# Kernel optimization log

Measured on AMD Instinct MI355X. Metric: run time of the kernel, lower is better.

## Reference

```python
import jax, jax.numpy as jnp
import numpy as np
import math

B, L, D = 4, 4096, 1024
PI = math.pi
LN_EPS = 1e-5


def setup_inputs() -> dict:
    key = jax.random.key(0)
    ks = jax.random.split(key, 16)
    s = 1.0 / math.sqrt(D)
    inp = {
        "x": jax.random.normal(ks[0], (B, L, D), dtype=jnp.float32),
        # Linear weights stored as [in, out] (torch W.T)
        "Wk": jax.random.normal(ks[1], (D, D), dtype=jnp.float32) * s,
        "bk": jnp.zeros((D,), dtype=jnp.float32),
        "Wq": jax.random.normal(ks[2], (D, D), dtype=jnp.float32) * s,
        "bq": jnp.zeros((D,), dtype=jnp.float32),
        "Wv": jax.random.normal(ks[3], (D, D), dtype=jnp.float32) * s,
        "bv": jnp.zeros((D,), dtype=jnp.float32),
        "ln_g": jnp.ones((D,), dtype=jnp.float32),
        "ln_b": jnp.zeros((D,), dtype=jnp.float32),
        "Wo": jax.random.normal(ks[4], (D, D), dtype=jnp.float32) * s,
        "bo": jnp.zeros((D,), dtype=jnp.float32),
        "Wg1": jax.random.normal(ks[5], (D, D // 4), dtype=jnp.float32) * s,
        "bg1": jnp.zeros((D // 4,), dtype=jnp.float32),
        "Wg2": jax.random.normal(ks[6], (D // 4, 1), dtype=jnp.float32) * (2.0 / math.sqrt(D)),
        "bg2": jnp.zeros((1,), dtype=jnp.float32),
        "pos_phases": jax.random.normal(ks[7], (L, D), dtype=jnp.float32) * PI,
    }
    return inp


def _layernorm(x, g, b):
    mu = jnp.mean(x, axis=-1, keepdims=True)
    var = jnp.var(x, axis=-1, keepdims=True)
    return (x - mu) * jax.lax.rsqrt(var + LN_EPS) * g + b


def reference(x, Wk, bk, Wq, bq, Wv, bv, ln_g, ln_b, Wo, bo, Wg1, bg1, Wg2, bg2, pos_phases):
    # dropout is identity in eval mode
    key_phases = jnp.tanh(x @ Wk + bk) * PI          # [B,L,D]
    query_phases = jnp.tanh(x @ Wq + bq) * PI        # [B,L,D]
    V = x @ Wv + bv                                   # [B,L,D]

    cos_k, sin_k = jnp.cos(key_phases), jnp.sin(key_phases)
    cos_q, sin_q = jnp.cos(query_phases), jnp.sin(query_phases)

    mem_real = jnp.cumsum(V * cos_k, axis=1)
    mem_imag = jnp.cumsum(V * sin_k, axis=1)
    content_retrieved = mem_real * cos_q + mem_imag * sin_q

    pp = pos_phases[: x.shape[1]]                     # [L,D]
    cos_p, sin_p = jnp.cos(pp), jnp.sin(pp)
    pos_mem_real = jnp.cumsum(V * cos_p, axis=1)
    pos_mem_imag = jnp.cumsum(V * sin_p, axis=1)
    pos_retrieved = pos_mem_real * cos_p + pos_mem_imag * sin_p

    gate = jax.nn.sigmoid(jax.nn.gelu(x @ Wg1 + bg1) @ Wg2 + bg2)  # [B,L,1]
    combined = gate * content_retrieved + (1.0 - gate) * pos_retrieved

    positions = jnp.arange(1, x.shape[1] + 1, dtype=jnp.float32)
    norm = jnp.sqrt(positions)[None, :, None]
    out = _layernorm(combined / norm, ln_g, ln_b) @ Wo + bo
    return x + out
```

## Files before the change

kernel.cpp:

```cpp
#include <hip/hip_runtime.h>
#include <math.h>

#define B_ 4
#define L_ 4096
#define D_ 1024
#define DG_ 256
#define NC_ 256
#define CL_ 16
#define SEGL_ 8
#define NSEG_ 32
#define PI_F 3.14159265358979323846f
#define LN_EPS_F 1e-5f

typedef __attribute__((ext_vector_type(8))) _Float16 f16x8;
typedef __attribute__((ext_vector_type(8))) short s16x8;
typedef __attribute__((ext_vector_type(4))) short s16x4;
typedef __attribute__((ext_vector_type(4))) float f32x4;

__device__ inline short f2h(float f) { return __builtin_bit_cast(short, (_Float16)f); }
__device__ inline float h2f(short s) { return (float)__builtin_bit_cast(_Float16, s); }

__device__ inline float ftanh(float x) {
    float e = __expf(2.0f * x);
    return 1.0f - 2.0f / (e + 1.0f);
}
__device__ inline void fsincos(float x, float* s, float* c) {
    *s = __sinf(x); *c = __cosf(x);
}

__device__ inline void gld16(const void* g, void* l) {
    __builtin_amdgcn_global_load_lds(
        (const __attribute__((address_space(1))) unsigned int*)g,
        (__attribute__((address_space(3))) unsigned int*)l, 16, 0, 0);
}

__global__ __launch_bounds__(256)
void conv_x(const float* __restrict__ x, short* __restrict__ xh, int n8)
{
    int t = blockIdx.x * 256 + threadIdx.x;
    if (t >= n8) return;
    const float4* p = (const float4*)x + (size_t)t * 2;
    float4 a = p[0], b = p[1];
    s16x8 v;
    v[0] = f2h(a.x); v[1] = f2h(a.y); v[2] = f2h(a.z); v[3] = f2h(a.w);
    v[4] = f2h(b.x); v[5] = f2h(b.y); v[6] = f2h(b.z); v[7] = f2h(b.w);
    *(s16x8*)(xh + (size_t)t * 8) = v;
}

__global__ __launch_bounds__(256)
void csp_kernel(const float* __restrict__ PP, short* __restrict__ CSP, int n4)
{
    int t = blockIdx.x * 256 + threadIdx.x;
    if (t >= n4) return;
    f32x4 p = *(const f32x4*)&PP[(size_t)t * 4];
    s16x8 o;
    #pragma unroll
    for (int j = 0; j < 4; ++j) {
        float s, c;
        fsincos(p[j], &s, &c);
        o[2 * j] = f2h(c);
        o[2 * j + 1] = f2h(s);
    }
    *(s16x8*)&CSP[(size_t)t * 8] = o;
}

__global__ __launch_bounds__(256)
void convT(const float* __restrict__ W, short* __restrict__ Th, int N)
{
    __shared__ float tile[64][65];
    const int n0 = blockIdx.x * 64, k0 = blockIdx.y * 64;
    const int t = threadIdx.x;
    const int r = t >> 4, c4 = (t & 15) * 4;

    #pragma unroll
    for (int i = 0; i < 4; ++i) {
        float4 v = *(const float4*)&W[(size_t)(k0 + r + i * 16) * N + n0 + c4];
        tile[r + i * 16][c4 + 0] = v.x;
        tile[r + i * 16][c4 + 1] = v.y;
        tile[r + i * 16][c4 + 2] = v.z;
        tile[r + i * 16][c4 + 3] = v.w;
    }
    __syncthreads();
    #pragma unroll
    for (int i = 0; i < 4; ++i) {
        const int n = r + i * 16;
        s16x4 o;
        o[0] = f2h(tile[c4 + 0][n]);
        o[1] = f2h(tile[c4 + 1][n]);
        o[2] = f2h(tile[c4 + 2][n]);
        o[3] = f2h(tile[c4 + 3][n]);
        *(s16x4*)&Th[(size_t)(n0 + n) * 1024 + k0 + c4] = o;
    }
}

#define BARRIER() __builtin_amdgcn_s_barrier()
#define PRIO1() __builtin_amdgcn_s_setprio(1)
#define PRIO0() __builtin_amdgcn_s_setprio(0)
#define LGKM0() do { asm volatile("s_waitcnt lgkmcnt(0)" ::: "memory"); \
                     __builtin_amdgcn_sched_barrier(0); } while (0)
#define VMC(N) asm volatile("s_waitcnt vmcnt(" #N ")" ::: "memory")

#define DSR(dst, areg, OFS)                                              \
    asm volatile("ds_read_b128 %0, %1 offset:" OFS                       \
                 : "=v"(dst) : "v"(areg))

#define RDA4(areg)                                                       \
    DSR(af[0], areg, "0");    DSR(af[1], areg, "2048");                  \
    DSR(af[2], areg, "4096"); DSR(af[3], areg, "6144");
#define RDA4H(areg)                                                      \
    DSR(af[0], areg, "8192");  DSR(af[1], areg, "10240");                \
    DSR(af[2], areg, "12288"); DSR(af[3], areg, "14336");
#define RDB4(areg, KK)                                                   \
    DSR(bq[0][KK], areg, "0");    DSR(bq[1][KK], areg, "2048");          \
    DSR(bq[2][KK], areg, "4096"); DSR(bq[3][KK], areg, "6144");

#define MF(MG, KK)                                                       \
    _Pragma("unroll") for (int i_ = 0; i_ < 4; ++i_)                     \
    _Pragma("unroll") for (int n_ = 0; n_ < 4; ++n_)                     \
        acc[(MG)*4 + i_][n_] = __builtin_amdgcn_mfma_f32_16x16x32_f16(   \
            af[i_], bq[n_][KK], acc[(MG)*4 + i_][n_], 0, 0, 0);

template<int EPI, typename OT>
__global__ __launch_bounds__(512, 2)
void mgemm256(const short* __restrict__ A, const short* __restrict__ Bt,
              const float* __restrict__ X, OT* __restrict__ out0,
              short* __restrict__ out1, short* __restrict__ out2,
              const float* __restrict__ b0, const float* __restrict__ b1,
              const float* __restrict__ b2, int M, int N, int K)
{
    extern __shared__ char lds[];

    const int tid = threadIdx.x;
    const int w = tid >> 6, l = tid & 63;
    const int wr = w >> 2, wc = w & 3;
    const int fr = l & 15, kb = l >> 4;
    const int bm = blockIdx.x * 256, bn = blockIdx.y * 256;
    const int np = K >> 7;

    const int s = fr & 7;
    const int cK0 = (((s >> 2) & 1) << 6) | (((kb ^ s) & 3) << 4);
    const int aA0 = (wr << 14) + fr * 128 + cK0;
    const int aA1 = aA0 ^ 64;
    const int aB0 = 32768 + ((wc >> 1) << 14) + ((wc & 1) * 64 + fr) * 128 + cK0;
    const int aB1 = aB0 ^ 64;
    const int aA0o = aA0 + 65536, aA1o = aA1 + 65536;
    const int aB0o = aB0 + 65536, aB1o = aB1 + 65536;

    const int p0 = tid * 16;
    const int sr = p0 >> 7;
    const int sc = (p0 & 127) ^ ((sr & 7) << 4);
    const short* gA = A  + (size_t)(bm + sr) * K + (sc >> 1);
    const short* gB = Bt + (size_t)(bn + sr) * K + (sc >> 1);
    char* ldst = lds + (w << 10);
    const size_t q1 = (size_t)64 * K, q2 = 2 * q1, q3 = 3 * q1;

    f32x4 acc[8][4] = {};
    f16x8 af[4];
    f16x8 bq[4][2];

    gld16(gA,      ldst);          gld16(gA + q1, ldst + 8192);
    gld16(gA + q2, ldst + 16384);  gld16(gA + q3, ldst + 24576);
    gld16(gB,      ldst + 32768);  gld16(gB + q1, ldst + 40960);
    gld16(gB + q2, ldst + 49152);  gld16(gB + q3, ldst + 57344);
    VMC(0);
    BARRIER();

    const short* gAn = gA + 64;
    const short* gBn = gB + 64;

    for (int pp = 0; pp < np; ++pp) {
        const bool nl = (pp + 1 < np);

        RDA4(aA0); RDB4(aB0, 0);
        gld16(gBn,      ldst + 98304);         gld16(gBn + q1, ldst + 98304 + 8192);
        gld16(gBn + q2, ldst + 98304 + 16384); gld16(gBn + q3, ldst + 98304 + 24576);
        LGKM0();
        PRIO1(); MF(0, 0); PRIO0();
        RDA4(aA1); RDB4(aB1, 1);
        gld16(gAn,      ldst + 65536);         gld16(gAn + q1, ldst + 65536 + 8192);
        gld16(gAn + q2, ldst + 65536 + 16384); gld16(gAn + q3, ldst + 65536 + 24576);
        LGKM0();
        PRIO1(); MF(0, 1); PRIO0();
        RDA4H(aA0);
        LGKM0();
        PRIO1(); MF(1, 0); PRIO0();
        RDA4H(aA1);
        LGKM0();
        PRIO1(); MF(1, 1); PRIO0();
        VMC(0);
        BARRIER();

        RDA4(aA0o); RDB4(aB0o, 0);
        if (nl) {
            gld16(gBn +      64, ldst + 32768); gld16(gBn + q1 + 64, ldst + 40960);
            gld16(gBn + q2 + 64, ldst + 49152); gld16(gBn + q3 + 64, ldst + 57344);
        }
        LGKM0();
        PRIO1(); MF(0, 0); PRIO0();
        RDA4(aA1o); RDB4(aB1o, 1);
        if (nl) {
            gld16(gAn +      64, ldst);         gld16(gAn + q1 + 64, ldst + 8192);
            gld16(gAn + q2 + 64, ldst + 16384); gld16(gAn + q3 + 64, ldst + 24576);
        }
        LGKM0();
        PRIO1(); MF(0, 1); PRIO0();
        RDA4H(aA0o);
        LGKM0();
        PRIO1(); MF(1, 0); PRIO0();
        RDA4H(aA1o);
        LGKM0();
        PRIO1(); MF(1, 1); PRIO0();
        if (nl) {
            VMC(0);
            BARRIER();
        }
        gAn += 128; gBn += 128;
    }

    if constexpr (EPI == 4) {
        short* op; const float* bp; bool dt;
        if (bn < 1024)      { op = (short*)out0; bp = b0; dt = true;  }
        else if (bn < 2048) { op = out1;         bp = b1; dt = true;  }
        else                { op = out2;         bp = b2; dt = false; }
        const int cb = bn & 1023;
        float bc[4];
        #pragma unroll
        for (int nf = 0; nf < 4; ++nf) bc[nf] = bp[cb + wc * 64 + nf * 16 + fr];
        #pragma unroll
        for (int mf = 0; mf < 8; ++mf)
            #pragma unroll
            for (int rr = 0; rr < 4; ++rr) {
                const int row = bm + wr * 128 + mf * 16 + kb * 4 + rr;
                #pragma unroll
                for (int nf = 0; nf < 4; ++nf) {
                    const int cc = cb + wc * 64 + nf * 16 + fr;
                    float c = acc[mf][nf][rr] + bc[nf];
                    if (dt) c = ftanh(c) * PI_F;
                    op[(size_t)row * 1024 + cc] = f2h(c);
                }
            }
    } else {
        float bc[4];
        #pragma unroll
        for (int nf = 0; nf < 4; ++nf) bc[nf] = b0[bn + wc * 64 + nf * 16 + fr];
        #pragma unroll
        for (int mf = 0; mf < 8; ++mf)
            #pragma unroll
            for (int rr = 0; rr < 4; ++rr) {
                const int row = bm + wr * 128 + mf * 16 + kb * 4 + rr;
                #pragma unroll
                for (int nf = 0; nf < 4; ++nf) {
                    const int col = bn + wc * 64 + nf * 16 + fr;
                    float c = acc[mf][nf][rr] + bc[nf] + X[(size_t)row * N + col];
                    ((float*)out0)[(size_t)row * N + col] = c;
                }
            }
    }
}

#define RDAF(areg)                                                       \
    DSR(af[0], areg, "0");    DSR(af[1], areg, "2048");                  \
    DSR(af[2], areg, "4096"); DSR(af[3], areg, "6144");
#define RDBF(areg)                                                       \
    DSR(bqs[0], areg, "0");    DSR(bqs[1], areg, "2048");                \
    DSR(bqs[2], areg, "4096"); DSR(bqs[3], areg, "6144");

#define MF16()                                                           \
    _Pragma("unroll") for (int i_ = 0; i_ < 4; ++i_)                     \
    _Pragma("unroll") for (int n_ = 0; n_ < 4; ++n_)                     \
        acc[i_][n_] = __builtin_amdgcn_mfma_f32_16x16x32_f16(            \
            af[i_], bqs[n_], acc[i_][n_], 0, 0, 0);

template<int EPI>
__global__ __launch_bounds__(256, 2)
void gemm128(const short* __restrict__ A, const short* __restrict__ Bt,
             const float* __restrict__ b0, const float* __restrict__ wg2p,
             float* __restrict__ gatep, int M, int N, int K)
{
    extern __shared__ char lds[];

    const int tid = threadIdx.x;
    const int w = tid >> 6, l = tid & 63;
    const int wr = w >> 1, wc = w & 1;
    const int fr = l & 15, kb = l >> 4;
    const int bm = blockIdx.x * 128, bn = blockIdx.y * 128;

    const int s = fr & 7;
    const int cK0 = (((s >> 2) & 1) << 6) | (((kb ^ s) & 3) << 4);
    const int aA0e = (wr * 64 + fr) * 128 + cK0;
    const int aA1e = aA0e ^ 64;
    const int aB0e = 16384 + (wc * 64 + fr) * 128 + cK0;
    const int aB1e = aB0e ^ 64;
    const int aA0o = aA0e + 32768, aA1o = aA1e + 32768;
    const int aB0o = aB0e + 32768, aB1o = aB1e + 32768;

    const int p16 = tid * 16;
    const int sr = p16 >> 7;
    const int sc = (p16 & 127) ^ ((sr & 7) << 4);
    const short* gA = A  + (size_t)(bm + sr) * K + (sc >> 1);
    const short* gB = Bt + (size_t)(bn + sr) * K + (sc >> 1);
    char* ldA = lds + (w << 10);
    const size_t r32 = (size_t)32 * K;

    f32x4 acc[4][4] = {};
    f16x8 af[4], bqs[4];

    #pragma unroll
    for (int i = 0; i < 4; ++i) gld16(gA + i * r32, ldA + i * 4096);
    #pragma unroll
    for (int i = 0; i < 4; ++i) gld16(gB + i * r32, ldA + 16384 + i * 4096);
    VMC(0);
    BARRIER();

    const short* gAt = gA;
    const short* gBt = gB;
    const int np = K >> 7;

    for (int pp = 0; pp < np; ++pp) {
        const bool nl = (pp + 1 < np);

        RDAF(aA0e); RDBF(aB0e);
        #pragma unroll
        for (int i = 0; i < 4; ++i) gld16(gAt + 64 + i * r32, ldA + 32768 + i * 4096);
        LGKM0();
        PRIO1(); MF16(); PRIO0();
        RDAF(aA1e); RDBF(aB1e);
        #pragma unroll
        for (int i = 0; i < 4; ++i) gld16(gBt + 64 + i * r32, ldA + 49152 + i * 4096);
        LGKM0();
        PRIO1(); MF16(); PRIO0();
        VMC(0);
        BARRIER();

        RDAF(aA0o); RDBF(aB0o);
        if (nl) {
            #pragma unroll
            for (int i = 0; i < 4; ++i) gld16(gAt + 128 + i * r32, ldA + i * 4096);
        }
        LGKM0();
        PRIO1(); MF16(); PRIO0();
        RDAF(aA1o); RDBF(aB1o);
        if (nl) {
            #pragma unroll
            for (int i = 0; i < 4; ++i) gld16(gBt + 128 + i * r32, ldA + 16384 + i * 4096);
        }
        LGKM0();
        PRIO1(); MF16(); PRIO0();
        if (nl) {
            VMC(0);
            BARRIER();
        }
        gAt += 128; gBt += 128;
    }

    float bg[4], wg[4];
    #pragma unroll
    for (int nf = 0; nf < 4; ++nf) {
        const int cl = bn + wc * 64 + nf * 16 + fr;
        bg[nf] = b0[cl];
        wg[nf] = wg2p[cl];
    }
    #pragma unroll
    for (int mf = 0; mf < 4; ++mf)
        #pragma unroll
        for (int rr = 0; rr < 4; ++rr) {
            const int row = bm + wr * 64 + mf * 16 + kb * 4 + rr;
            float part = 0.f;
            #pragma unroll
            for (int nf = 0; nf < 4; ++nf) {
                float c = acc[mf][nf][rr] + bg[nf];
                float tt = 0.7978845608028654f * (c + 0.044715f * c * c * c);
                float g = 0.5f * c * (1.0f + ftanh(tt));
                part += g * wg[nf];
            }
            part += __shfl_xor(part, 1);
            part += __shfl_xor(part, 2);
            part += __shfl_xor(part, 4);
            part += __shfl_xor(part, 8);
            if (fr == 0) atomicAdd(&gatep[row], part);
        }
}

__global__ __launch_bounds__(256)
void passA(const short* __restrict__ V, const short* __restrict__ KP,
           const short* __restrict__ CSP, f32x4* __restrict__ SI)
{
    const int bid = blockIdx.x;
    const int b = bid >> 8, c = bid & 255;
    const int d0 = threadIdx.x * 4;

    f32x4 cr = {}, ci = {}, pr = {}, pi = {};
    const size_t base = ((size_t)b * L_ + (size_t)c * CL_) * D_ + d0;
    const size_t pcs  = ((size_t)c * CL_ * D_ + d0) * 2;
    for (int ll = 0; ll < CL_; ++ll) {
        s16x4 v4  = *(const s16x4*)&V [base + (size_t)ll * D_];
        s16x4 kp4 = *(const s16x4*)&KP[base + (size_t)ll * D_];
        s16x8 c8  = *(const s16x8*)&CSP[pcs + (size_t)ll * (D_ * 2)];
        #pragma unroll
        for (int j = 0; j < 4; ++j) {
            float v = h2f(v4[j]);
            float sk, ck;
            fsincos(h2f(kp4[j]), &sk, &ck);
            float cp = h2f(c8[2 * j]), sp = h2f(c8[2 * j + 1]);
            cr[j] += v * ck; ci[j] += v * sk;
            pr[j] += v * cp; pi[j] += v * sp;
        }
    }
    const size_t sidx = ((size_t)bid << 10) + d0;
    #pragma unroll
    for (int j = 0; j < 4; ++j) {
        f32x4 o = { cr[j], ci[j], pr[j], pi[j] };
        SI[sidx + j] = o;
    }
}

__global__ __launch_bounds__(256)
void passB1(f32x4* __restrict__ SI, f32x4* __restrict__ STS)
{
    const int seg = blockIdx.x & (NSEG_ - 1);
    const int t = (blockIdx.x >> 5) * 256 + threadIdx.x;
    const int b = t >> 10, d = t & 1023;
    f32x4 run = {};
    #pragma unroll
    for (int i = 0; i < SEGL_; ++i) {
        const int c = seg * SEGL_ + i;
        const size_t idx = ((size_t)(b * NC_ + c) << 10) + d;
        f32x4 v = SI[idx];
        SI[idx] = run;
        run += v;
    }
    STS[((size_t)(b * NSEG_ + seg) << 10) + d] = run;
}

__global__ __launch_bounds__(256)
void passB2(f32x4* __restrict__ STS)
{
    const int t = blockIdx.x * 256 + threadIdx.x;
    const int b = t >> 10, d = t & 1023;
    f32x4 run = {};
    #pragma unroll
    for (int seg = 0; seg < NSEG_; ++seg) {
        const size_t idx = ((size_t)(b * NSEG_ + seg) << 10) + d;
        f32x4 v = STS[idx];
        STS[idx] = run;
        run += v;
    }
}

__global__ __launch_bounds__(256)
void passC(const short* __restrict__ V, const short* KP,
           const short* __restrict__ QP, const short* __restrict__ CSP,
           const float* __restrict__ gatep, const float* __restrict__ bg2,
           const f32x4* __restrict__ SI, const f32x4* __restrict__ STS,
           const float* __restrict__ ln_g, const float* __restrict__ ln_b,
           short* Yb)
{
    const int w = threadIdx.x >> 6, lane = threadIdx.x & 63;
    const int gw = blockIdx.x * 4 + w;
    const int b = gw >> 8, c = gw & 255;
    const int d0 = lane * 16;

    const size_t sidx = ((size_t)gw << 10) + d0;
    const size_t tidx = ((size_t)(b * NSEG_ + (c >> 3)) << 10) + d0;
    float cr[16], ci[16], pr[16], pi[16];
    #pragma unroll
    for (int j = 0; j < 16; ++j) {
        f32x4 s0 = SI[sidx + j] + STS[tidx + j];
        cr[j] = s0[0]; ci[j] = s0[1]; pr[j] = s0[2]; pi[j] = s0[3];
    }
    float gl[16], bl[16];
    #pragma unroll
    for (int j = 0; j < 16; ++j) { gl[j] = ln_g[d0 + j]; bl[j] = ln_b[d0 + j]; }
    const float bg2v = bg2[0];

    const int lbase = c * CL_;
    size_t off = ((size_t)b * L_ + lbase) * D_ + d0;
    size_t cso = ((size_t)lbase * D_ + d0) * 2;

    s16x8 v8a, v8b, k8a, k8b, q8a, q8b, c8a, c8b, c8c, c8d;
    v8a = *(const s16x8*)&V [off];      v8b = *(const s16x8*)&V [off + 8];
    k8a = *(const s16x8*)&KP[off];      k8b = *(const s16x8*)&KP[off + 8];
    q8a = *(const s16x8*)&QP[off];      q8b = *(const s16x8*)&QP[off + 8];
    c8a = *(const s16x8*)&CSP[cso];     c8b = *(const s16x8*)&CSP[cso + 8];
    c8c = *(const s16x8*)&CSP[cso + 16];c8d = *(const s16x8*)&CSP[cso + 24];
    float gpre = gatep[b * L_ + lbase];

    for (int l0 = 0; l0 < CL_; ++l0) {
        const int ll = lbase + l0;
        const size_t offn = off + D_;
        const size_t cson = cso + D_ * 2;
        s16x8 v8an = v8a, v8bn = v8b, k8an = k8a, k8bn = k8b;
        s16x8 q8an = q8a, q8bn = q8b, c8an = c8a, c8bn = c8b, c8cn = c8c, c8dn = c8d;
        float gpn = gpre;
        if (l0 + 1 < CL_) {
            v8an = *(const s16x8*)&V [offn];      v8bn = *(const s16x8*)&V [offn + 8];
            k8an = *(const s16x8*)&KP[offn];      k8bn = *(const s16x8*)&KP[offn + 8];
            q8an = *(const s16x8*)&QP[offn];      q8bn = *(const s16x8*)&QP[offn + 8];
            c8an = *(const s16x8*)&CSP[cson];     c8bn = *(const s16x8*)&CSP[cson + 8];
            c8cn = *(const s16x8*)&CSP[cson + 16];c8dn = *(const s16x8*)&CSP[cson + 24];
            gpn  = gatep[b * L_ + ll + 1];
        }

        const float gv = 1.0f / (1.0f + __expf(-(gpre + bg2v)));
        const float rs_pos = rsqrtf((float)(ll + 1));

        float u[16];
        float sm = 0.f, s2 = 0.f;
        #pragma unroll
        for (int j = 0; j < 16; ++j) {
            const short vs = (j < 8) ? v8a[j & 7] : v8b[j & 7];
            const short ks = (j < 8) ? k8a[j & 7] : k8b[j & 7];
            const short qs = (j < 8) ? q8a[j & 7] : q8b[j & 7];
            const int cj = 2 * j;
            const short cps = (cj < 8) ? c8a[cj & 7]
                             : (cj < 16) ? c8b[cj & 7]
                             : (cj < 24) ? c8c[cj & 7] : c8d[cj & 7];
            const short sps = (cj + 1 < 8) ? c8a[(cj + 1) & 7]
                             : (cj + 1 < 16) ? c8b[(cj + 1) & 7]
                             : (cj + 1 < 24) ? c8c[(cj + 1) & 7] : c8d[(cj + 1) & 7];
            float v = h2f(vs);
            float sk, ck, sq, cq;
            fsincos(h2f(ks), &sk, &ck);
            fsincos(h2f(qs), &sq, &cq);
            float cp = h2f(cps), sp = h2f(sps);
            cr[j] += v * ck; ci[j] += v * sk;
            pr[j] += v * cp; pi[j] += v * sp;
            float content = cr[j] * cq + ci[j] * sq;
            float posr    = pr[j] * cp + pi[j] * sp;
            u[j] = (gv * content + (1.0f - gv) * posr) * rs_pos;
            sm += u[j]; s2 += u[j] * u[j];
        }

        #pragma unroll
        for (int o = 32; o; o >>= 1) {
            sm += __shfl_down(sm, o);
            s2 += __shfl_down(s2, o);
        }
        sm = __shfl(sm, 0);
        s2 = __shfl(s2, 0);
        const float mu  = sm * (1.0f / D_);
        const float var = s2 * (1.0f / D_) - mu * mu;
        const float rsv = rsqrtf(var + LN_EPS_F);
        s16x8 yo0, yo1;
        #pragma unroll
        for (int j = 0; j < 8; ++j)
            yo0[j] = f2h((u[j] - mu) * rsv * gl[j] + bl[j]);
        #pragma unroll
        for (int j = 0; j < 8; ++j)
            yo1[j] = f2h((u[8 + j] - mu) * rsv * gl[8 + j] + bl[8 + j]);
        *(s16x8*)&Yb[off] = yo0;
        *(s16x8*)&Yb[off + 8] = yo1;

        off = offn; cso = cson;
        v8a = v8an; v8b = v8bn; k8a = k8an; k8b = k8bn;
        q8a = q8an; q8b = q8bn;
        c8a = c8an; c8b = c8bn; c8c = c8cn; c8d = c8dn;
        gpre = gpn;
    }
}

extern "C" void kernel_launch(void* const* d_in, const int* in_sizes, int n_in,
                              void* d_out, int out_size, void* d_ws, size_t ws_size,
                              hipStream_t stream)
{
    const float* x    = (const float*)d_in[0];
    const float* Wk   = (const float*)d_in[1];
    const float* bk   = (const float*)d_in[2];
    const float* Wq   = (const float*)d_in[3];
    const float* bq   = (const float*)d_in[4];
    const float* Wv   = (const float*)d_in[5];
    const float* bv   = (const float*)d_in[6];
    const float* ln_g = (const float*)d_in[7];
    const float* ln_b = (const float*)d_in[8];
    const float* Wo   = (const float*)d_in[9];
    const float* bo   = (const float*)d_in[10];
    const float* Wg1  = (const float*)d_in[11];
    const float* bg1  = (const float*)d_in[12];
    const float* Wg2  = (const float*)d_in[13];
    const float* bg2  = (const float*)d_in[14];
    const float* PP   = (const float*)d_in[15];

    float* out = (float*)d_out;

    const size_t BLD   = (size_t)B_ * L_ * D_;
    const size_t SZ_X  = BLD * 2;
    const size_t SZ_R1 = (size_t)B_ * L_ * DG_ * 2;
    const size_t SZ_G1 = (size_t)D_ * DG_ * 2;
    const size_t SZ_GT = (size_t)B_ * L_ * 4;
    const size_t NEED  = SZ_X + SZ_R1 + SZ_G1 + 3 * SZ_X + SZ_GT;
    if (ws_size < NEED) {
        hipMemcpyAsync(d_out, d_in[0], BLD * sizeof(float),
                       hipMemcpyDeviceToDevice, stream);
        return;
    }

    char* wsb = (char*)d_ws;
    short* xh   = (short*)(wsb);
    char*  r1   = wsb + SZ_X;
    short* Wcat = (short*)r1;
    short* Wg1T = (short*)(r1 + SZ_R1);
    short* KP   = (short*)(r1 + SZ_R1 + SZ_G1);
    short* QP   = (short*)((char*)KP + SZ_X);
    short* V    = (short*)((char*)QP + SZ_X);
    float* gatep = (float*)((char*)V + SZ_X);
    f32x4* SI   = (f32x4*)(wsb);
    short* CSP  = (short*)(wsb + 16777216);
    short* WtO  = (short*)r1;
    f32x4* STS  = (f32x4*)(r1 + 2097152);
    short* Yb   = KP;

    const int M = B_ * L_;
    dim3 blk(256);

    conv_x<<<(int)(BLD / 8 / 256), blk, 0, stream>>>(x, xh, (int)(BLD / 8));
    dim3 gT(D_ / 64, 16);
    dim3 gTg(DG_ / 64, 16);
    convT<<<gT, blk, 0, stream>>>(Wk, Wcat + (size_t)0 * D_ * D_, D_);
    convT<<<gT, blk, 0, stream>>>(Wq, Wcat + (size_t)1 * D_ * D_, D_);
    convT<<<gT, blk, 0, stream>>>(Wv, Wcat + (size_t)2 * D_ * D_, D_);
    convT<<<gTg, blk, 0, stream>>>(Wg1, Wg1T, DG_);
    hipMemsetAsync(gatep, 0, SZ_GT, stream);

    dim3 gQKV(M / 256, 3072 / 256);
    hipLaunchKernelGGL((mgemm256<4, short>), gQKV, dim3(512), 131072, stream,
                       xh, Wcat, nullptr, KP, QP, V, bk, bq, bv, M, 3072, D_);
    dim3 gH(M / 128, DG_ / 128);
    hipLaunchKernelGGL((gemm128<5>), gH, blk, 65536, stream,
                       xh, Wg1T, bg1, Wg2, gatep, M, DG_, D_);

    convT<<<gT, blk, 0, stream>>>(Wo, WtO, D_);
    csp_kernel<<<(int)((size_t)L_ * D_ / 4 / 256), blk, 0, stream>>>(
        PP, CSP, (int)((size_t)L_ * D_ / 4));

    passA<<<B_ * NC_, blk, 0, stream>>>(V, KP, CSP, SI);
    passB1<<<(B_ * D_ / 256) * NSEG_, blk, 0, stream>>>(SI, STS);
    passB2<<<B_ * D_ / 256, blk, 0, stream>>>(STS);
    passC<<<B_ * NC_ / 4, blk, 0, stream>>>(V, KP, QP, CSP, gatep, bg2, SI, STS,
                                            ln_g, ln_b, Yb);

    dim3 gO(M / 256, D_ / 256);
    hipLaunchKernelGGL((mgemm256<3, float>), gO, dim3(512), 131072, stream,
                       Yb, WtO, x, out, nullptr, nullptr, bo, nullptr, nullptr,
                       M, D_, D_);
}
```

Before: 282.6 us.

## Reorder GEMM main loop for finer-grained load/compute overlap with partial vmcnt waits

Restructures the double-buffered MFMA main loop so each K-half reuses one set of B fragments across both M groups, instead of holding two K-halves of B in registers. Global-to-LDS loads are split into pairs interleaved with the MFMA groups, and the single full vmcnt(0) wait per half-iteration becomes several vmcnt(2) waits plus barriers. This aims to cut register pressure and hide load latency better. The cost is more barriers per iteration and a more delicate ordering of load completion against LDS reads.

```diff
diff --git a/kernel.cpp b/kernel.cpp
--- a/kernel.cpp
+++ b/kernel.cpp
@@ -110,15 +110,15 @@
 #define RDA4H(areg)                                                      \
     DSR(af[0], areg, "8192");  DSR(af[1], areg, "10240");                \
     DSR(af[2], areg, "12288"); DSR(af[3], areg, "14336");
-#define RDB4(areg, KK)                                                   \
-    DSR(bq[0][KK], areg, "0");    DSR(bq[1][KK], areg, "2048");          \
-    DSR(bq[2][KK], areg, "4096"); DSR(bq[3][KK], areg, "6144");
-
-#define MF(MG, KK)                                                       \
+#define RDB4S(areg)                                                      \
+    DSR(bq[0], areg, "0");    DSR(bq[1], areg, "2048");                  \
+    DSR(bq[2], areg, "4096"); DSR(bq[3], areg, "6144");
+
+#define MF2(MG)                                                          \
     _Pragma("unroll") for (int i_ = 0; i_ < 4; ++i_)                     \
     _Pragma("unroll") for (int n_ = 0; n_ < 4; ++n_)                     \
         acc[(MG)*4 + i_][n_] = __builtin_amdgcn_mfma_f32_16x16x32_f16(   \
-            af[i_], bq[n_][KK], acc[(MG)*4 + i_][n_], 0, 0, 0);
+            af[i_], bq[n_], acc[(MG)*4 + i_][n_], 0, 0, 0);
 
 template<int EPI, typename OT>
 __global__ __launch_bounds__(512, 2)
@@ -156,7 +156,7 @@
 
     f32x4 acc[8][4] = {};
     f16x8 af[4];
-    f16x8 bq[4][2];
+    f16x8 bq[4];
 
     gld16(gA,      ldst);          gld16(gA + q1, ldst + 8192);
     gld16(gA + q2, ldst + 16384);  gld16(gA + q3, ldst + 24576);
@@ -171,49 +171,56 @@
     for (int pp = 0; pp < np; ++pp) {
         const bool nl = (pp + 1 < np);
 
-        RDA4(aA0); RDB4(aB0, 0);
+        VMC(2);
+        BARRIER();
+        RDA4(aA0); RDB4S(aB0);
         gld16(gBn,      ldst + 98304);         gld16(gBn + q1, ldst + 98304 + 8192);
+        LGKM0();
+        PRIO1(); MF2(0); PRIO0();
+        VMC(2);
+        BARRIER();
+        RDA4H(aA0);
         gld16(gBn + q2, ldst + 98304 + 16384); gld16(gBn + q3, ldst + 98304 + 24576);
         LGKM0();
-        PRIO1(); MF(0, 0); PRIO0();
-        RDA4(aA1); RDB4(aB1, 1);
-        gld16(gAn,      ldst + 65536);         gld16(gAn + q1, ldst + 65536 + 8192);
-        gld16(gAn + q2, ldst + 65536 + 16384); gld16(gAn + q3, ldst + 65536 + 24576);
-        LGKM0();
-        PRIO1(); MF(0, 1); PRIO0();
-        RDA4H(aA0);
-        LGKM0();
-        PRIO1(); MF(1, 0); PRIO0();
+        PRIO1(); MF2(1); PRIO0();
+        RDA4(aA1); RDB4S(aB1);
+        gld16(gAn,      ldst + 65536);         gld16(gAn + q2, ldst + 65536 + 16384);
+        LGKM0();
+        PRIO1(); MF2(0); PRIO0();
         RDA4H(aA1);
-        LGKM0();
-        PRIO1(); MF(1, 1); PRIO0();
-        VMC(0);
+        gld16(gAn + q1, ldst + 65536 + 8192);  gld16(gAn + q3, ldst + 65536 + 24576);
+        LGKM0();
+        PRIO1(); MF2(1); PRIO0();
+
+        VMC(2);
         BARRIER();
-
-        RDA4(aA0o); RDB4(aB0o, 0);
+        RDA4(aA0o); RDB4S(aB0o);
         if (nl) {
             gld16(gBn +      64, ldst + 32768); gld16(gBn + q1 + 64, ldst + 40960);
+        }
+        LGKM0();
+        PRIO1(); MF2(0); PRIO0();
+        if (nl) { VMC(2); } else { VMC(0); }
+        BARRIER();
+        RDA4H(aA0o);
+        if (nl) {
             gld16(gBn + q2 + 64, ldst + 49152); gld16(gBn + q3 + 64, ldst + 57344);
         }
         LGKM0();
-        PRIO1(); MF(0, 0); PRIO0();
-        RDA4(aA1o); RDB4(aB1o, 1);
+        PRIO1(); MF2(1); PRIO0();
+        RDA4(aA1o); RDB4S(aB1o);
         if (nl) {
-            gld16(gAn +      64, ldst);         gld16(gAn + q1 + 64, ldst + 8192);
-            gld16(gAn + q2 + 64, ldst + 16384); gld16(gAn + q3 + 64, ldst + 24576);
-        }
-        LGKM0();
-        PRIO1(); MF(0, 1); PRIO0();
-        RDA4H(aA0o);
-        LGKM0();
-        PRIO1(); MF(1, 0); PRIO0();
+            gld16(gAn +      64, ldst);         gld16(gAn + q2 + 64, ldst + 16384);
+        }
+        LGKM0();
+        PRIO1(); MF2(0); PRIO0();
         RDA4H(aA1o);
-        LGKM0();
-        PRIO1(); MF(1, 1); PRIO0();
         if (nl) {
-            VMC(0);
-            BARRIER();
-        }
+            gld16(gAn + q1 + 64, ldst + 8192);  gld16(gAn + q3 + 64, ldst + 24576);
+        }
+        LGKM0();
+        PRIO1(); MF2(1); PRIO0();
+
         gAn += 128; gBn += 128;
     }
 
```

Measured after the change: 393.2 us. 1.39x slower.
